# Kernel optimization log

Hardware: AMD Instinct MI355X
Metric: run time of the kernel (lower is better)

Reference implementation:

```python
import jax, jax.numpy as jnp
import numpy as np

B, T, H, P = 256, 512, 512, 128


def _lstm_cell(x, h, c, Wih, Whh, bih, bhh):
    # torch.nn.LSTMCell math: gates = x@Wih^T + bih + h@Whh^T + bhh, chunks i,f,g,o
    gates = x @ Wih.T + h @ Whh.T + (bih + bhh)
    i, f, g, o = jnp.split(gates, 4, axis=-1)
    c2 = jax.nn.sigmoid(f) * c + jax.nn.sigmoid(i) * jnp.tanh(g)
    h2 = jax.nn.sigmoid(o) * jnp.tanh(c2)
    return h2, c2


def setup_inputs() -> dict:
    key = jax.random.key(0)
    ks = jax.random.split(key, 12)
    s = 0.1
    return {
        "x": jax.random.normal(ks[0], (B, T), dtype=jnp.float32),
        "enc_Wih": jax.random.normal(ks[1], (4 * H, 1), dtype=jnp.float32) * s,
        "enc_Whh": jax.random.normal(ks[2], (4 * H, H), dtype=jnp.float32) * s,
        "enc_bih": jax.random.normal(ks[3], (4 * H,), dtype=jnp.float32) * s,
        "enc_bhh": jax.random.normal(ks[4], (4 * H,), dtype=jnp.float32) * s,
        "dec_Wih": jax.random.normal(ks[5], (4 * H, H), dtype=jnp.float32) * s,
        "dec_Whh": jax.random.normal(ks[6], (4 * H, H), dtype=jnp.float32) * s,
        "dec_bih": jax.random.normal(ks[7], (4 * H,), dtype=jnp.float32) * s,
        "dec_bhh": jax.random.normal(ks[8], (4 * H,), dtype=jnp.float32) * s,
        "dense_W": jax.random.normal(ks[9], (1, H), dtype=jnp.float32) * s,
        "dense_b": jax.random.normal(ks[10], (1,), dtype=jnp.float32) * s,
        "predict_length": P,
    }


def reference(x, enc_Wih, enc_Whh, enc_bih, enc_bhh,
              dec_Wih, dec_Whh, dec_bih, dec_bhh,
              dense_W, dense_b, predict_length):
    batch = x.shape[0]
    x3 = x[:, :, None]  # [B, T, 1]
    h0 = jnp.zeros((batch, H), dtype=x.dtype)
    c0 = jnp.zeros((batch, H), dtype=x.dtype)

    # Encoder: scan over time
    def enc_step(carry, xt):
        h, c = carry
        h, c = _lstm_cell(xt, h, c, enc_Wih, enc_Whh, enc_bih, enc_bhh)
        return (h, c), None

    (h, c), _ = jax.lax.scan(enc_step, (h0, c0), jnp.transpose(x3, (1, 0, 2)))

    # Decoder loop (faithful to original: decoder state updated but unused for x;
    # encoder is re-run from the frozen (h, c) each step)
    def dec_step(carry, _):
        xc, nh, nc = carry
        nh2, nc2 = _lstm_cell(xc, nh, nc, dec_Wih, dec_Whh, dec_bih, dec_bhh)
        y = xc @ dense_W.T + dense_b            # [B, 1]
        x_next, _ = _lstm_cell(y, h, c, enc_Wih, enc_Whh, enc_bih, enc_bhh)
        return (x_next, nh2, nc2), y

    _, ys = jax.lax.scan(dec_step, (h, h, c), None, length=predict_length)
    # ys: [P, B, 1] -> [B, P]
    return jnp.transpose(ys[:, :, 0], (1, 0))
```

## Files before the change

kernel.cpp:

```cpp
#include <hip/hip_runtime.h>

#define B_ 256
#define T_ 512
#define H_ 512
#define P_ 128
#define G4 2048

typedef __attribute__((ext_vector_type(8))) _Float16 h8_t;
typedef __attribute__((ext_vector_type(4))) float floatx4;

__device__ __forceinline__ float sigm(float x){ return 1.0f / (1.0f + __expf(-x)); }
__device__ __forceinline__ float tanh_(float x){ return 2.0f / (1.0f + __expf(-2.0f*x)) - 1.0f; }
__device__ __forceinline__ unsigned short f2h(float f){
  union { _Float16 h; unsigned short u; } c; c.h = (_Float16)f; return c.u;
}
__device__ __forceinline__ float wredsum(float v){
  #pragma unroll
  for (int off = 32; off; off >>= 1) v += __shfl_xor(v, off, 64);
  return v;
}

__global__ __launch_bounds__(256) void pack_w(const float* __restrict__ Whh,
                                              unsigned short* __restrict__ Wp){
  int p8   = blockIdx.x * 256 + threadIdx.x;
  int lane = p8 & 63;
  int kt   = (p8 >> 6) & 15;
  int ct   = (p8 >> 10) & 1;
  int w    = (p8 >> 11) & 3;
  int cg   = (p8 >> 13) & 15;
  int q    = (lane & 15) >> 2, dhc = lane & 3;
  int col  = q*512 + cg*32 + w*8 + ct*4 + dhc;
  int k0   = kt*32 + (lane >> 4)*8;
  const float* s = Whh + (size_t)col * H_ + k0;
  unsigned short v[8];
  #pragma unroll
  for (int e = 0; e < 8; e++) v[e] = f2h(s[e]);
  *(uint4*)(Wp + (size_t)p8 * 8) = *(const uint4*)v;
}

__global__ __launch_bounds__(256) void enc_persist(
    const unsigned short* __restrict__ Wp,
    const float* __restrict__ x,
    const float* __restrict__ Wih,
    const float* __restrict__ bih,
    const float* __restrict__ bhh,
    unsigned long long* __restrict__ D,
    unsigned long long* __restrict__ S,
    float* __restrict__ hfp,
    float* __restrict__ cfin,
    float* __restrict__ G,
    int zf)
{
  __shared__ float x_lds[16][512];
  __shared__ uint4 A_lds4[1024];
  __shared__ float Sg[4][16][33];
  __shared__ char pad_[30000];

  char* A_lds = (char*)A_lds4;
  const int bid = blockIdx.x;
  const int tid = threadIdx.x;
  const int lane = tid & 63, wv = tid >> 6;

  if (zf){ pad_[tid] = (char)Wih[tid]; if (!tid) A_lds[0] = pad_[128]; }

  const int g  = bid >> 4;
  const int cg = bid & 15;

  h8_t wreg[2][16];
  {
    const unsigned short* wb = Wp + (size_t)((cg*4 + wv)*2) * 8192;
    #pragma unroll
    for (int ct = 0; ct < 2; ct++)
      #pragma unroll
      for (int kt = 0; kt < 16; kt++)
        wreg[ct][kt] = *(const h8_t*)(wb + (ct*16 + kt)*512 + lane*8);
  }
  #pragma unroll
  for (int i = 0; i < 8; i++){
    int idx = tid + i*256;
    int r = idx >> 7, c4 = (idx & 127)*4;
    *(float4*)&x_lds[r][c4] = *(const float4*)&x[(size_t)(g*16 + r)*T_ + c4];
  }
  const int erow = tid >> 4;
  const int hp   = tid & 15;
  const int hc0  = cg*32 + hp*2;
  float wih0[4], wih1[4], bs0[4], bs1[4];
  #pragma unroll
  for (int q = 0; q < 4; q++){
    wih0[q] = Wih[q*512 + hc0];     wih1[q] = Wih[q*512 + hc0 + 1];
    bs0[q]  = bih[q*512 + hc0]     + bhh[q*512 + hc0];
    bs1[q]  = bih[q*512 + hc0 + 1] + bhh[q*512 + hc0 + 1];
  }
  float cr0 = 0.f, cr1 = 0.f;

  const int rxor_st = (erow & 7) << 4;
  const size_t Dg = (size_t)g * 2048;
  const size_t pidx = Dg + (size_t)erow*128 + cg*8 + (hp >> 1);
  const int arow = lane & 15, ahalf = lane >> 4;
  const int rxor = (arow & 7) << 4;

  for (int t = 0; t <= T_; t++){
    const int rpar = (t + 1) & 1;
    if (tid < 16){
      const unsigned long long want = (unsigned long long)t;
      while (__hip_atomic_load(S + rpar*256 + g*16 + tid, __ATOMIC_RELAXED,
                               __HIP_MEMORY_SCOPE_AGENT) != want)
        ;
    }
    __syncthreads();
    {
      const unsigned long long* Db = D + (size_t)rpar*32768 + Dg
                                       + (size_t)erow*128 + hp;
      unsigned long long wbuf[8];
      #pragma unroll
      for (int wi = 0; wi < 8; wi++)
        wbuf[wi] = __hip_atomic_load(Db + wi*16, __ATOMIC_RELAXED,
                                     __HIP_MEMORY_SCOPE_AGENT);
      #pragma unroll
      for (int wi = 0; wi < 8; wi++)
        *(unsigned long long*)(A_lds + erow*1024 + ((hp*8 + wi*128) ^ rxor_st))
            = wbuf[wi];
    }
    __syncthreads();

    floatx4 acc0 = {0,0,0,0}, acc1 = {0,0,0,0};
    h8_t a[16];
    #pragma unroll
    for (int kt = 0; kt < 16; kt++)
      a[kt] = *(const h8_t*)(A_lds + arow*1024 + ((kt*64 + ahalf*16) ^ rxor));
    #pragma unroll
    for (int kt = 0; kt < 16; kt++){
      acc0 = __builtin_amdgcn_mfma_f32_16x16x32_f16(a[kt], wreg[0][kt], acc0, 0,0,0);
      acc1 = __builtin_amdgcn_mfma_f32_16x16x32_f16(a[kt], wreg[1][kt], acc1, 0,0,0);
    }
    #pragma unroll
    for (int r = 0; r < 4; r++){
      int srow = ahalf*4 + r;
      int q = (lane & 15) >> 2, dhc = lane & 3;
      Sg[q][srow][wv*8 + dhc]     = acc0[r];
      Sg[q][srow][wv*8 + 4 + dhc] = acc1[r];
    }
    __syncthreads();

    if (t == T_){
      int b = g*16 + erow;
      #pragma unroll
      for (int q = 0; q < 4; q++){
        G[(size_t)b*G4 + q*512 + hc0]     = Sg[q][erow][hp*2]     + bs0[q];
        G[(size_t)b*G4 + q*512 + hc0 + 1] = Sg[q][erow][hp*2 + 1] + bs1[q];
      }
      break;
    }

    const float xb = x_lds[erow][t];
    float pi0 = Sg[0][erow][hp*2] + xb*wih0[0] + bs0[0];
    float pf0 = Sg[1][erow][hp*2] + xb*wih0[1] + bs0[1];
    float pg0 = Sg[2][erow][hp*2] + xb*wih0[2] + bs0[2];
    float po0 = Sg[3][erow][hp*2] + xb*wih0[3] + bs0[3];
    float c20 = sigm(pf0)*cr0 + sigm(pi0)*tanh_(pg0);
    float h0  = sigm(po0)*tanh_(c20);  cr0 = c20;

    float pi1 = Sg[0][erow][hp*2+1] + xb*wih1[0] + bs1[0];
    float pf1 = Sg[1][erow][hp*2+1] + xb*wih1[1] + bs1[1];
    float pg1 = Sg[2][erow][hp*2+1] + xb*wih1[2] + bs1[2];
    float po1 = Sg[3][erow][hp*2+1] + xb*wih1[3] + bs1[3];
    float c21 = sigm(pf1)*cr1 + sigm(pi1)*tanh_(pg1);
    float h1  = sigm(po1)*tanh_(c21);  cr1 = c21;

    unsigned pay = (unsigned)f2h(h0) | ((unsigned)f2h(h1) << 16);
    unsigned payN = __shfl_xor(pay, 1);
    const int wpar = t & 1;
    if (!(hp & 1)){
      unsigned long long wo = (unsigned long long)pay
                            | ((unsigned long long)payN << 32);
      (void)__hip_atomic_exchange(D + (size_t)wpar*32768 + pidx, wo,
                                  __ATOMIC_RELAXED, __HIP_MEMORY_SCOPE_AGENT);
    }
    asm volatile("s_waitcnt vmcnt(0)" ::: "memory");
    __syncthreads();
    if (tid == 0)
      (void)__hip_atomic_exchange(S + wpar*256 + g*16 + cg,
                                  (unsigned long long)(t + 1),
                                  __ATOMIC_RELAXED, __HIP_MEMORY_SCOPE_AGENT);

    if (t == T_-1){
      int b = g*16 + erow;
      hfp[(size_t)b*512 + hc0]     = h0;  hfp[(size_t)b*512 + hc0 + 1] = h1;
      cfin[(size_t)b*512 + hc0]    = c20; cfin[(size_t)b*512 + hc0 + 1] = c21;
    }
  }
}

__global__ __launch_bounds__(256) void decoder(
    const float* __restrict__ G, const float* __restrict__ c,
    const float* __restrict__ hfp, const float* __restrict__ Wih,
    const float* __restrict__ dW, const float* __restrict__ db,
    float* __restrict__ out)
{
  const int row  = blockIdx.x * 4 + (threadIdx.x >> 6);
  const int lane = threadIdx.x & 63;
  float Gr[4][8], wr[4][8], cc[8], wd[8];
  float p = 0.f;
  #pragma unroll
  for (int k = 0; k < 8; k++){
    int j = lane + k*64;
    cc[k] = c[(size_t)row*H_ + j];
    wd[k] = dW[j];
    #pragma unroll
    for (int q = 0; q < 4; q++){
      Gr[q][k] = G[(size_t)row*G4 + q*512 + j];
      wr[q][k] = Wih[q*512 + j];
    }
    p += hfp[(size_t)row*H_ + j] * wd[k];
  }
  const float bias = db[0];
  float y = wredsum(p) + bias;
  for (int tt = 0; tt < P_; tt++){
    if (lane == 0) out[(size_t)row*P_ + tt] = y;
    if (tt == P_-1) break;
    float pp = 0.f;
    #pragma unroll
    for (int k = 0; k < 8; k++){
      float i_ = sigm (y*wr[0][k] + Gr[0][k]);
      float f_ = sigm (y*wr[1][k] + Gr[1][k]);
      float g_ = tanh_(y*wr[2][k] + Gr[2][k]);
      float o_ = sigm (y*wr[3][k] + Gr[3][k]);
      float c2 = f_*cc[k] + i_*g_;
      pp += o_*tanh_(c2)*wd[k];
    }
    y = wredsum(pp) + bias;
  }
}

extern "C" void kernel_launch(void* const* d_in, const int* in_sizes, int n_in,
                              void* d_out, int out_size, void* d_ws, size_t ws_size,
                              hipStream_t stream)
{
  const float* x    = (const float*)d_in[0];
  const float* Wih  = (const float*)d_in[1];
  const float* Whh  = (const float*)d_in[2];
  const float* bih  = (const float*)d_in[3];
  const float* bhh  = (const float*)d_in[4];
  const float* dW   = (const float*)d_in[9];
  const float* db   = (const float*)d_in[10];
  float* out = (float*)d_out;

  unsigned short* Wp    = (unsigned short*)d_ws;
  unsigned long long* D = (unsigned long long*)(Wp + 1048576);
  unsigned long long* S = D + 65536;
  float* hfp  = (float*)(S + 512);
  float* cfin = hfp + 131072;
  float* G    = cfin + 131072;

  hipMemsetAsync(D, 0, (65536 + 512) * sizeof(unsigned long long), stream);
  pack_w<<<512, 256, 0, stream>>>(Whh, Wp);
  enc_persist<<<256, 256, 0, stream>>>(Wp, x, Wih, bih, bhh, D, S,
                                       hfp, cfin, G, 0);
  decoder<<<64, 256, 0, stream>>>(G, cfin, hfp, Wih, dW, db, out);
}
```

Measured before the change: 1.557 ms.

## Interleave two batch groups per persistent encoder block to hide sync latency

The persistent encoder now runs 128 blocks instead of 256, and each block handles two 16-row batch groups with the same column slice of weights. Each timestep runs the two groups one after the other, so while one group's exchange settles the block computes the other. Both step flags are published once per timestep. The LDS padding trick is dropped because it is no longer needed. This halves the number of blocks that must spin-wait together, at the cost of running each step's work serially inside one block.

New measurement: 2.589 ms. 1.66x slower.

```diff
diff --git a/kernel.cpp b/kernel.cpp
--- a/kernel.cpp
+++ b/kernel.cpp
@@ -8,6 +8,7 @@
 
 typedef __attribute__((ext_vector_type(8))) _Float16 h8_t;
 typedef __attribute__((ext_vector_type(4))) float floatx4;
+typedef unsigned long long ull;
 
 __device__ __forceinline__ float sigm(float x){ return 1.0f / (1.0f + __expf(-x)); }
 __device__ __forceinline__ float tanh_(float x){ return 2.0f / (1.0f + __expf(-2.0f*x)) - 1.0f; }
@@ -44,27 +45,24 @@
     const float* __restrict__ Wih,
     const float* __restrict__ bih,
     const float* __restrict__ bhh,
-    unsigned long long* __restrict__ D,
-    unsigned long long* __restrict__ S,
+    ull* __restrict__ D,
+    ull* __restrict__ S,
     float* __restrict__ hfp,
     float* __restrict__ cfin,
-    float* __restrict__ G,
-    int zf)
+    float* __restrict__ G)
 {
-  __shared__ float x_lds[16][512];
+  __shared__ float x_lds[32][512];
   __shared__ uint4 A_lds4[1024];
   __shared__ float Sg[4][16][33];
-  __shared__ char pad_[30000];
 
   char* A_lds = (char*)A_lds4;
   const int bid = blockIdx.x;
   const int tid = threadIdx.x;
   const int lane = tid & 63, wv = tid >> 6;
 
-  if (zf){ pad_[tid] = (char)Wih[tid]; if (!tid) A_lds[0] = pad_[128]; }
-
-  const int g  = bid >> 4;
+  const int p  = bid >> 4;
   const int cg = bid & 15;
+  const int gA = p*2, gB = p*2 + 1;
 
   h8_t wreg[2][16];
   {
@@ -76,10 +74,10 @@
         wreg[ct][kt] = *(const h8_t*)(wb + (ct*16 + kt)*512 + lane*8);
   }
   #pragma unroll
-  for (int i = 0; i < 8; i++){
+  for (int i = 0; i < 16; i++){
     int idx = tid + i*256;
     int r = idx >> 7, c4 = (idx & 127)*4;
-    *(float4*)&x_lds[r][c4] = *(const float4*)&x[(size_t)(g*16 + r)*T_ + c4];
+    *(float4*)&x_lds[r][c4] = *(const float4*)&x[(size_t)(p*32 + r)*T_ + c4];
   }
   const int erow = tid >> 4;
   const int hp   = tid & 15;
@@ -91,35 +89,32 @@
     bs0[q]  = bih[q*512 + hc0]     + bhh[q*512 + hc0];
     bs1[q]  = bih[q*512 + hc0 + 1] + bhh[q*512 + hc0 + 1];
   }
-  float cr0 = 0.f, cr1 = 0.f;
+  float crA0 = 0.f, crA1 = 0.f, crB0 = 0.f, crB1 = 0.f;
 
   const int rxor_st = (erow & 7) << 4;
-  const size_t Dg = (size_t)g * 2048;
-  const size_t pidx = Dg + (size_t)erow*128 + cg*8 + (hp >> 1);
   const int arow = lane & 15, ahalf = lane >> 4;
   const int rxor = (arow & 7) << 4;
 
-  for (int t = 0; t <= T_; t++){
+  auto phase = [&](int g, int xbase, float& cr0, float& cr1, int t){
     const int rpar = (t + 1) & 1;
     if (tid < 16){
-      const unsigned long long want = (unsigned long long)t;
+      const ull want = (ull)t;
       while (__hip_atomic_load(S + rpar*256 + g*16 + tid, __ATOMIC_RELAXED,
                                __HIP_MEMORY_SCOPE_AGENT) != want)
         ;
     }
     __syncthreads();
     {
-      const unsigned long long* Db = D + (size_t)rpar*32768 + Dg
-                                       + (size_t)erow*128 + hp;
-      unsigned long long wbuf[8];
+      const ull* Db = D + (size_t)rpar*32768 + (size_t)g*2048
+                        + (size_t)erow*128 + hp;
+      ull wbuf[8];
       #pragma unroll
       for (int wi = 0; wi < 8; wi++)
         wbuf[wi] = __hip_atomic_load(Db + wi*16, __ATOMIC_RELAXED,
                                      __HIP_MEMORY_SCOPE_AGENT);
       #pragma unroll
       for (int wi = 0; wi < 8; wi++)
-        *(unsigned long long*)(A_lds + erow*1024 + ((hp*8 + wi*128) ^ rxor_st))
-            = wbuf[wi];
+        *(ull*)(A_lds + erow*1024 + ((hp*8 + wi*128) ^ rxor_st)) = wbuf[wi];
     }
     __syncthreads();
 
@@ -142,17 +137,17 @@
     }
     __syncthreads();
 
+    int b = g*16 + erow;
     if (t == T_){
-      int b = g*16 + erow;
       #pragma unroll
       for (int q = 0; q < 4; q++){
         G[(size_t)b*G4 + q*512 + hc0]     = Sg[q][erow][hp*2]     + bs0[q];
         G[(size_t)b*G4 + q*512 + hc0 + 1] = Sg[q][erow][hp*2 + 1] + bs1[q];
       }
-      break;
-    }
-
-    const float xb = x_lds[erow][t];
+      return;
+    }
+
+    const float xb = x_lds[xbase + erow][t];
     float pi0 = Sg[0][erow][hp*2] + xb*wih0[0] + bs0[0];
     float pf0 = Sg[1][erow][hp*2] + xb*wih0[1] + bs0[1];
     float pg0 = Sg[2][erow][hp*2] + xb*wih0[2] + bs0[2];
@@ -167,26 +162,33 @@
     float c21 = sigm(pf1)*cr1 + sigm(pi1)*tanh_(pg1);
     float h1  = sigm(po1)*tanh_(c21);  cr1 = c21;
 
+    if (t == T_-1){
+      hfp[(size_t)b*512 + hc0]     = h0;  hfp[(size_t)b*512 + hc0 + 1] = h1;
+      cfin[(size_t)b*512 + hc0]    = c20; cfin[(size_t)b*512 + hc0 + 1] = c21;
+    }
     unsigned pay = (unsigned)f2h(h0) | ((unsigned)f2h(h1) << 16);
     unsigned payN = __shfl_xor(pay, 1);
-    const int wpar = t & 1;
     if (!(hp & 1)){
-      unsigned long long wo = (unsigned long long)pay
-                            | ((unsigned long long)payN << 32);
-      (void)__hip_atomic_exchange(D + (size_t)wpar*32768 + pidx, wo,
+      ull wo = (ull)pay | ((ull)payN << 32);
+      (void)__hip_atomic_exchange(D + (size_t)(t & 1)*32768 + (size_t)g*2048
+                                    + (size_t)erow*128 + cg*8 + (hp >> 1),
+                                  wo, __ATOMIC_RELAXED,
+                                  __HIP_MEMORY_SCOPE_AGENT);
+    }
+  };
+
+  for (int t = 0; t <= T_; t++){
+    phase(gA, 0,  crA0, crA1, t);
+    phase(gB, 16, crB0, crB1, t);
+    if (t == T_) break;
+    asm volatile("s_waitcnt vmcnt(0)" ::: "memory");
+    __syncthreads();
+    if (tid == 0){
+      const int wpar = t & 1;
+      (void)__hip_atomic_exchange(S + wpar*256 + gA*16 + cg, (ull)(t + 1),
                                   __ATOMIC_RELAXED, __HIP_MEMORY_SCOPE_AGENT);
-    }
-    asm volatile("s_waitcnt vmcnt(0)" ::: "memory");
-    __syncthreads();
-    if (tid == 0)
-      (void)__hip_atomic_exchange(S + wpar*256 + g*16 + cg,
-                                  (unsigned long long)(t + 1),
+      (void)__hip_atomic_exchange(S + wpar*256 + gB*16 + cg, (ull)(t + 1),
                                   __ATOMIC_RELAXED, __HIP_MEMORY_SCOPE_AGENT);
-
-    if (t == T_-1){
-      int b = g*16 + erow;
-      hfp[(size_t)b*512 + hc0]     = h0;  hfp[(size_t)b*512 + hc0 + 1] = h1;
-      cfin[(size_t)b*512 + hc0]    = c20; cfin[(size_t)b*512 + hc0 + 1] = c21;
     }
   }
 }
@@ -245,16 +247,16 @@
   const float* db   = (const float*)d_in[10];
   float* out = (float*)d_out;
 
-  unsigned short* Wp    = (unsigned short*)d_ws;
-  unsigned long long* D = (unsigned long long*)(Wp + 1048576);
-  unsigned long long* S = D + 65536;
+  unsigned short* Wp = (unsigned short*)d_ws;
+  ull* D = (ull*)(Wp + 1048576);
+  ull* S = D + 65536;
   float* hfp  = (float*)(S + 512);
   float* cfin = hfp + 131072;
   float* G    = cfin + 131072;
 
-  hipMemsetAsync(D, 0, (65536 + 512) * sizeof(unsigned long long), stream);
+  hipMemsetAsync(D, 0, (65536 + 512) * sizeof(ull), stream);
   pack_w<<<512, 256, 0, stream>>>(Whh, Wp);
-  enc_persist<<<256, 256, 0, stream>>>(Wp, x, Wih, bih, bhh, D, S,
-                                       hfp, cfin, G, 0);
+  enc_persist<<<128, 256, 0, stream>>>(Wp, x, Wih, bih, bhh, D, S,
+                                       hfp, cfin, G);
   decoder<<<64, 256, 0, stream>>>(G, cfin, hfp, Wih, dW, db, out);
 }
```
